# Optimization experiments

Measured on AMD Instinct MI355X. Metric: run time of the kernel, lower is better.

Reference implementation:

```python
import jax, jax.numpy as jnp
import numpy as np

N = 20000      # num nodes
E = 320000     # num edges
F = 128        # num_features
NUM_RBF = 20   # Message.num_atoms (hardcoded in torch source)
CUTOFF = 5.0


def setup_inputs() -> dict:
    key = jax.random.key(0)
    ks = jax.random.split(key, 12)
    node_s = jax.random.normal(ks[0], (N, F), dtype=jnp.float32)
    node_vec = jax.random.normal(ks[1], (N, F, 3), dtype=jnp.float32)
    edge = jax.random.randint(ks[2], (E, 2), 0, N, dtype=jnp.int32)
    edge_difference = jax.random.normal(ks[3], (E, 3), dtype=jnp.float32)
    # distances strictly positive and mostly inside cutoff (rbf divides by dist)
    edge_dis = jax.random.uniform(ks[4], (E,), dtype=jnp.float32, minval=0.5, maxval=CUTOFF * 1.1)
    s = 1.0 / np.sqrt(F)
    W1 = jax.random.normal(ks[5], (F, F), dtype=jnp.float32) * s
    b1 = jnp.zeros((F,), dtype=jnp.float32)
    W2 = jax.random.normal(ks[6], (F, 3 * F), dtype=jnp.float32) * s
    b2 = jnp.zeros((3 * F,), dtype=jnp.float32)
    Wf = jax.random.normal(ks[7], (NUM_RBF, 3 * F), dtype=jnp.float32) / np.sqrt(NUM_RBF)
    bf = jnp.zeros((3 * F,), dtype=jnp.float32)
    return {"node_s": node_s, "node_vec": node_vec, "edge": edge,
            "edge_difference": edge_difference, "edge_dis": edge_dis,
            "W1": W1, "b1": b1, "W2": W2, "b2": b2, "Wf": Wf, "bf": bf}


def reference(node_s, node_vec, edge, edge_difference, edge_dis, W1, b1, W2, b2, Wf, bf):
    src = edge[:, 1]  # gather index (neighbor j)
    dst = edge[:, 0]  # scatter index (center i)
    inv_d = 1.0 / edge_dis[:, None]                                   # [E,1]
    n = jnp.arange(1, NUM_RBF + 1, dtype=edge_dis.dtype)              # [20]
    rbf_feat = jnp.sin((n * (jnp.pi / CUTOFF)) * edge_dis[:, None]) * inv_d  # [E,20]
    filt = rbf_feat @ Wf + bf                                         # [E,3F]
    ccut = jnp.where(edge_dis <= CUTOFF,
                     0.5 * (jnp.cos(jnp.pi * edge_dis / CUTOFF) + 1.0), 0.0)  # [E]
    # faithful to torch: both filter and cutoff are re-indexed by edge[:,1]
    filter_W = filt[src] * ccut[src][:, None]                         # [E,3F]
    h = jax.nn.silu(node_s @ W1 + b1)                                 # [N,F]
    s_out = h @ W2 + b2                                               # [N,3F]
    filer_output = filter_W * s_out[src]                              # [E,3F]
    gate_state, gate_edge, message_scalar = jnp.split(filer_output, 3, axis=1)
    message_vec = node_vec[src] * gate_state[:, :, None]              # [E,F,3]
    # edge_vec in the torch source is dead code (never used) -> omitted
    temp_s = jnp.zeros_like(node_s).at[dst].add(message_scalar)       # [N,F]
    temp_vec = jnp.zeros_like(node_vec).at[dst].add(message_vec)      # [N,F,3]
    return (node_vec + temp_vec, node_s + temp_s)
```

## Files before the change

### kernel.cpp

```cpp
#include <hip/hip_runtime.h>
#include <hip/hip_bf16.h>

#define FDIM 128
#define NRBF 20
#define PI_OVER_CUT 0.6283185307179586f

#define WCONV_ELEMS (128 * 128 + 256 * 128 + 256 * 32)
#define WCONV_BLOCKS (WCONV_ELEMS / 256)

#define DEG_CAP 64

#define EPB 1024

typedef short bf8_t __attribute__((ext_vector_type(8)));
typedef float f4_t  __attribute__((ext_vector_type(4)));
typedef unsigned short us8_t __attribute__((ext_vector_type(8)));

static __device__ __forceinline__ unsigned short bf16_bits(float x) {
    unsigned u = __float_as_uint(x);
    unsigned r = u + 0x7FFF + ((u >> 16) & 1);
    return (unsigned short)(r >> 16);
}
static __device__ __forceinline__ float bf16_f(unsigned short b) {
    return __uint_as_float(((unsigned)b) << 16);
}

__global__ __launch_bounds__(256) void prep_kernel(
    const float* __restrict__ W1, const float* __restrict__ W2,
    const float* __restrict__ Wf,
    unsigned short* __restrict__ W1T, unsigned short* __restrict__ W2T,
    unsigned short* __restrict__ WfT,
    int* __restrict__ cursor, int N)
{
    int b = blockIdx.x;
    if (b < WCONV_BLOCKS) {
        int i = b * 256 + threadIdx.x;
        if (i < 128 * 128) {
            int n = i >> 7, k = i & 127;
            W1T[n * 128 + k] = bf16_bits(W1[k * 128 + n]);
        } else if (i < 128 * 128 + 256 * 128) {
            int j = i - 128 * 128;
            int n = j >> 7, k = j & 127;
            int col = (n < 128) ? n : n + 128;
            W2T[n * 128 + k] = bf16_bits(W2[k * 384 + col]);
        } else {
            int j = i - (128 * 128 + 256 * 128);
            int n = j >> 5, k = j & 31;
            int col = (n < 128) ? n : n + 128;
            WfT[n * 32 + k] = (k < NRBF) ? bf16_bits(Wf[k * 384 + col])
                                         : (unsigned short)0;
        }
    } else {
        int i = (b - WCONV_BLOCKS) * 256 + threadIdx.x;
        if (i < N) cursor[i] = 0;
    }
}

__global__ __launch_bounds__(256) void node_fused(
    const float* __restrict__ S, const float* __restrict__ node_vec,
    const float* __restrict__ edge_dis,
    const unsigned short* __restrict__ W1T, const float* __restrict__ b1,
    const unsigned short* __restrict__ W2T, const float* __restrict__ b2,
    const unsigned short* __restrict__ WfT, const float* __restrict__ bfv,
    ushort4* __restrict__ VM, int N,
    const int* __restrict__ edge, int* __restrict__ cursor,
    int* __restrict__ src_pad, int E, int edgeBlocks)
{
    if (blockIdx.x < edgeBlocks) {
        int base = blockIdx.x * EPB;
        #pragma unroll
        for (int it = 0; it < 4; it++) {
            int i = base + it * 256 + threadIdx.x;
            if (i < E) {
                int2 e = ((const int2*)edge)[i];
                int pos = atomicAdd(&cursor[e.x], 1);
                src_pad[((size_t)e.x << 6) + pos] = e.y;
            }
        }
        return;
    }

    __shared__ __align__(16) unsigned short sh_s[16][136];
    __shared__ __align__(16) unsigned short sh_h[16][136];
    __shared__ __align__(16) unsigned short sh_rbf[16][40];
    __shared__ float sh_ccut[16];

    const int tid  = threadIdx.x;
    const int lane = tid & 63;
    const int wave = tid >> 6;
    const int l15  = lane & 15;
    const int quad = lane >> 4;
    const int m0   = (blockIdx.x - edgeBlocks) * 16;

    for (int t = tid; t < 16 * 32; t += 256) {
        int row = t >> 5, c4 = (t & 31) * 4;
        int n = m0 + row; if (n >= N) n = N - 1;
        float4 x = *(const float4*)(S + (size_t)n * FDIM + c4);
        ushort4 u;
        u.x = bf16_bits(x.x); u.y = bf16_bits(x.y);
        u.z = bf16_bits(x.z); u.w = bf16_bits(x.w);
        *(ushort4*)&sh_s[row][c4] = u;
    }
    if (tid < 16 * 8) {
        int row = tid >> 3, k0 = (tid & 7) * 4;
        int n = m0 + row; if (n >= N) n = N - 1;
        float dd = edge_dis[n];
        float ph = PI_OVER_CUT * dd;
        float inv = 1.0f / dd;
        ushort4 u;
        u.x = (k0 + 0 < NRBF) ? bf16_bits(sinf((float)(k0 + 1) * ph) * inv) : 0;
        u.y = (k0 + 1 < NRBF) ? bf16_bits(sinf((float)(k0 + 2) * ph) * inv) : 0;
        u.z = (k0 + 2 < NRBF) ? bf16_bits(sinf((float)(k0 + 3) * ph) * inv) : 0;
        u.w = (k0 + 3 < NRBF) ? bf16_bits(sinf((float)(k0 + 4) * ph) * inv) : 0;
        *(ushort4*)&sh_rbf[row][k0] = u;
    }
    if (tid < 16) {
        int n = m0 + tid; if (n >= N) n = N - 1;
        float dd = edge_dis[n];
        sh_ccut[tid] = (dd <= 5.0f) ? 0.5f * (cosf(PI_OVER_CUT * dd) + 1.0f) : 0.0f;
    }
    __syncthreads();

    {
        bf8_t a1[4];
        #pragma unroll
        for (int kk = 0; kk < 4; kk++)
            a1[kk] = *(const bf8_t*)&sh_s[l15][kk * 32 + quad * 8];

        #pragma unroll
        for (int i = 0; i < 2; i++) {
            int col = (wave * 2 + i) * 16 + l15;
            const unsigned short* wp = W1T + (size_t)col * FDIM + quad * 8;
            f4_t acc = {0.f, 0.f, 0.f, 0.f};
            #pragma unroll
            for (int kk = 0; kk < 4; kk++) {
                bf8_t b = *(const bf8_t*)(wp + kk * 32);
                acc = __builtin_amdgcn_mfma_f32_16x16x32_bf16(a1[kk], b, acc, 0, 0, 0);
            }
            float bb = b1[col];
            #pragma unroll
            for (int r = 0; r < 4; r++) {
                float x = acc[r] + bb;
                x = x / (1.f + expf(-x));
                sh_h[quad * 4 + r][col] = bf16_bits(x);
            }
        }
    }
    __syncthreads();

    bf8_t a2[4], af;
    #pragma unroll
    for (int kk = 0; kk < 4; kk++)
        a2[kk] = *(const bf8_t*)&sh_h[l15][kk * 32 + quad * 8];
    af = *(const bf8_t*)&sh_rbf[l15][quad * 8];

    #pragma unroll
    for (int i = 0; i < 2; i++) {
        int pc = (wave * 2 + i) * 16 + l15;
        const unsigned short* wg = W2T + (size_t)pc * FDIM + quad * 8;
        const unsigned short* wm = W2T + (size_t)(pc + 128) * FDIM + quad * 8;
        f4_t ag = {0.f, 0.f, 0.f, 0.f}, am = {0.f, 0.f, 0.f, 0.f};
        #pragma unroll
        for (int kk = 0; kk < 4; kk++) {
            bf8_t bg = *(const bf8_t*)(wg + kk * 32);
            bf8_t bm = *(const bf8_t*)(wm + kk * 32);
            ag = __builtin_amdgcn_mfma_f32_16x16x32_bf16(a2[kk], bg, ag, 0, 0, 0);
            am = __builtin_amdgcn_mfma_f32_16x16x32_bf16(a2[kk], bm, am, 0, 0, 0);
        }
        f4_t fg = {0.f, 0.f, 0.f, 0.f}, fm = {0.f, 0.f, 0.f, 0.f};
        {
            bf8_t bg = *(const bf8_t*)(WfT + (size_t)pc * 32 + quad * 8);
            bf8_t bm = *(const bf8_t*)(WfT + (size_t)(pc + 128) * 32 + quad * 8);
            fg = __builtin_amdgcn_mfma_f32_16x16x32_bf16(af, bg, fg, 0, 0, 0);
            fm = __builtin_amdgcn_mfma_f32_16x16x32_bf16(af, bm, fm, 0, 0, 0);
        }

        float b2g = b2[pc], b2m = b2[256 + pc];
        float bfg = bfv[pc], bfm = bfv[256 + pc];
        #pragma unroll
        for (int r = 0; r < 4; r++) {
            int lrow = quad * 4 + r;
            int n = m0 + lrow;
            if (n < N) {
                float cc = sh_ccut[lrow];
                float a  = (fg[r] + bfg) * cc * (ag[r] + b2g);
                float mv = (fm[r] + bfm) * cc * (am[r] + b2m);
                const float* vp = node_vec + (size_t)n * 384 + 3 * pc;
                ushort4 rec;
                rec.x = bf16_bits(a * vp[0]);
                rec.y = bf16_bits(a * vp[1]);
                rec.z = bf16_bits(a * vp[2]);
                rec.w = bf16_bits(mv);
                VM[(size_t)n * FDIM + pc] = rec;
            }
        }
    }
}

__global__ __launch_bounds__(256) void gather_bf16(
    const int* __restrict__ cursor, const int* __restrict__ src_pad,
    const us8_t* __restrict__ VM8, const float* __restrict__ node_vec,
    const float* __restrict__ node_s,
    float* __restrict__ out_vec, float* __restrict__ out_s, int N)
{
    const int lane = threadIdx.x & 63;
    const int nw = gridDim.x * 4;
    for (int d = blockIdx.x * 4 + (threadIdx.x >> 6); d < N; d += nw) {
        int beg = d << 6;
        int end = beg + cursor[d];

        float a0A = 0.f, a1A = 0.f, a2A = 0.f, asA = 0.f;
        float a0B = 0.f, a1B = 0.f, a2B = 0.f, asB = 0.f;

        int j = beg;
        for (; j + 7 < end; j += 8) {
            us8_t r0 = VM8[(size_t)src_pad[j]     * 64 + lane];
            us8_t r1 = VM8[(size_t)src_pad[j + 1] * 64 + lane];
            us8_t r2 = VM8[(size_t)src_pad[j + 2] * 64 + lane];
            us8_t r3 = VM8[(size_t)src_pad[j + 3] * 64 + lane];
            us8_t r4 = VM8[(size_t)src_pad[j + 4] * 64 + lane];
            us8_t r5 = VM8[(size_t)src_pad[j + 5] * 64 + lane];
            us8_t r6 = VM8[(size_t)src_pad[j + 6] * 64 + lane];
            us8_t r7 = VM8[(size_t)src_pad[j + 7] * 64 + lane];
            #define ACC(r) \
                a0A += bf16_f(r[0]); a1A += bf16_f(r[1]); a2A += bf16_f(r[2]); asA += bf16_f(r[3]); \
                a0B += bf16_f(r[4]); a1B += bf16_f(r[5]); a2B += bf16_f(r[6]); asB += bf16_f(r[7]);
            ACC(r0) ACC(r1) ACC(r2) ACC(r3) ACC(r4) ACC(r5) ACC(r6) ACC(r7)
        }
        for (; j + 3 < end; j += 4) {
            us8_t r0 = VM8[(size_t)src_pad[j]     * 64 + lane];
            us8_t r1 = VM8[(size_t)src_pad[j + 1] * 64 + lane];
            us8_t r2 = VM8[(size_t)src_pad[j + 2] * 64 + lane];
            us8_t r3 = VM8[(size_t)src_pad[j + 3] * 64 + lane];
            ACC(r0) ACC(r1) ACC(r2) ACC(r3)
        }
        for (; j < end; j++) {
            us8_t r = VM8[(size_t)src_pad[j] * 64 + lane];
            ACC(r)
            #undef ACC
        }

        {
            const float* sp = node_s + (size_t)d * FDIM + 2 * lane;
            float* op = out_s + (size_t)d * FDIM + 2 * lane;
            float2 ns = *(const float2*)sp;
            float2 r; r.x = ns.x + asA; r.y = ns.y + asB;
            *(float2*)op = r;
        }
        {
            const float* ip = node_vec + (size_t)d * 384 + 6 * lane;
            float* op = out_vec + (size_t)d * 384 + 6 * lane;
            op[0] = ip[0] + a0A;
            op[1] = ip[1] + a1A;
            op[2] = ip[2] + a2A;
            op[3] = ip[3] + a0B;
            op[4] = ip[4] + a1B;
            op[5] = ip[5] + a2B;
        }
    }
}

extern "C" void kernel_launch(void* const* d_in, const int* in_sizes, int n_in,
                              void* d_out, int out_size, void* d_ws, size_t ws_size,
                              hipStream_t stream) {
    const float* node_s   = (const float*)d_in[0];
    const float* node_vec = (const float*)d_in[1];
    const int*   edge     = (const int*)d_in[2];
    const float* edge_dis = (const float*)d_in[4];
    const float* W1 = (const float*)d_in[5];
    const float* b1 = (const float*)d_in[6];
    const float* W2 = (const float*)d_in[7];
    const float* b2 = (const float*)d_in[8];
    const float* Wf = (const float*)d_in[9];
    const float* bf = (const float*)d_in[10];

    const int N = in_sizes[0] / FDIM;
    const int E = in_sizes[2] / 2;

    float* out_vec = (float*)d_out;
    float* out_s   = out_vec + (size_t)N * 384;

    int* cursor  = (int*)d_ws;
    int* src_pad = cursor + N;
    size_t int_bytes = (((size_t)N * (DEG_CAP + 1) * 4) + 15) & ~(size_t)15;
    unsigned short* W1T = (unsigned short*)((char*)d_ws + int_bytes);
    unsigned short* W2T = W1T + 128 * 128;
    unsigned short* WfT = W2T + 256 * 128;
    ushort4*        VMh = (ushort4*)(WfT + 256 * 32);

    const int zeroBlocks = (N + 255) / 256;
    prep_kernel<<<WCONV_BLOCKS + zeroBlocks, 256, 0, stream>>>(
        W1, W2, Wf, W1T, W2T, WfT, cursor, N);

    const int nodeBlocks = (N + 15) / 16;
    const int edgeBlocks = (E + EPB - 1) / EPB;
    node_fused<<<edgeBlocks + nodeBlocks, 256, 0, stream>>>(
        node_s, node_vec, edge_dis, W1T, b1, W2T, b2, WfT, bf, VMh, N,
        edge, cursor, src_pad, E, edgeBlocks);

    int gblocks = (N + 3) / 4;
    if (gblocks > 2048) gblocks = 2048;
    gather_bf16<<<gblocks, 256, 0, stream>>>(
        cursor, src_pad, (const us8_t*)VMh, node_vec, node_s,
        out_vec, out_s, N);
}
```

Measured before the change: 194.8 us.

## Merge prep, node and gather kernels into one cooperative persistent kernel

```diff
diff --git a/kernel.cpp b/kernel.cpp
--- a/kernel.cpp
+++ b/kernel.cpp
@@ -1,5 +1,8 @@
 #include <hip/hip_runtime.h>
+#include <hip/hip_cooperative_groups.h>
 #include <hip/hip_bf16.h>
+
+namespace cg = cooperative_groups;
 
 #define FDIM 128
 #define NRBF 20
@@ -25,72 +28,71 @@
     return __uint_as_float(((unsigned)b) << 16);
 }
 
-__global__ __launch_bounds__(256) void prep_kernel(
+struct NodeShared {
+    alignas(16) unsigned short sh_s[16][136];
+    alignas(16) unsigned short sh_h[16][136];
+    alignas(16) unsigned short sh_rbf[16][40];
+    alignas(16) float sh_ccut[16];
+};
+
+
+static __device__ __forceinline__ void do_prep_elem(
+    int i,
     const float* __restrict__ W1, const float* __restrict__ W2,
     const float* __restrict__ Wf,
     unsigned short* __restrict__ W1T, unsigned short* __restrict__ W2T,
     unsigned short* __restrict__ WfT,
     int* __restrict__ cursor, int N)
 {
-    int b = blockIdx.x;
-    if (b < WCONV_BLOCKS) {
-        int i = b * 256 + threadIdx.x;
-        if (i < 128 * 128) {
-            int n = i >> 7, k = i & 127;
-            W1T[n * 128 + k] = bf16_bits(W1[k * 128 + n]);
-        } else if (i < 128 * 128 + 256 * 128) {
-            int j = i - 128 * 128;
-            int n = j >> 7, k = j & 127;
-            int col = (n < 128) ? n : n + 128;
-            W2T[n * 128 + k] = bf16_bits(W2[k * 384 + col]);
-        } else {
-            int j = i - (128 * 128 + 256 * 128);
-            int n = j >> 5, k = j & 31;
-            int col = (n < 128) ? n : n + 128;
-            WfT[n * 32 + k] = (k < NRBF) ? bf16_bits(Wf[k * 384 + col])
-                                         : (unsigned short)0;
-        }
+    if (i < 128 * 128) {
+        int n = i >> 7, k = i & 127;
+        W1T[n * 128 + k] = bf16_bits(W1[k * 128 + n]);
+    } else if (i < 128 * 128 + 256 * 128) {
+        int j = i - 128 * 128;
+        int n = j >> 7, k = j & 127;
+        int col = (n < 128) ? n : n + 128;
+        W2T[n * 128 + k] = bf16_bits(W2[k * 384 + col]);
+    } else if (i < WCONV_ELEMS) {
+        int j = i - (128 * 128 + 256 * 128);
+        int n = j >> 5, k = j & 31;
+        int col = (n < 128) ? n : n + 128;
+        WfT[n * 32 + k] = (k < NRBF) ? bf16_bits(Wf[k * 384 + col])
+                                     : (unsigned short)0;
     } else {
-        int i = (b - WCONV_BLOCKS) * 256 + threadIdx.x;
-        if (i < N) cursor[i] = 0;
-    }
-}
-
-__global__ __launch_bounds__(256) void node_fused(
+        int d = i - WCONV_ELEMS;
+        if (d < N) cursor[d] = 0;
+    }
+}
+
+static __device__ __forceinline__ void do_edge_chunk(
+    int base, const int* __restrict__ edge, int E,
+    int* __restrict__ cursor, int* __restrict__ src_pad)
+{
+    #pragma unroll
+    for (int it = 0; it < 4; it++) {
+        int i = base + it * 256 + threadIdx.x;
+        if (i < E) {
+            int2 e = ((const int2*)edge)[i];
+            int pos = atomicAdd(&cursor[e.x], 1);
+            src_pad[((size_t)e.x << 6) + pos] = e.y;
+        }
+    }
+}
+
+static __device__ __forceinline__ void do_node_tile(
+    int m0, NodeShared& sh,
     const float* __restrict__ S, const float* __restrict__ node_vec,
     const float* __restrict__ edge_dis,
     const unsigned short* __restrict__ W1T, const float* __restrict__ b1,
     const unsigned short* __restrict__ W2T, const float* __restrict__ b2,
     const unsigned short* __restrict__ WfT, const float* __restrict__ bfv,
-    ushort4* __restrict__ VM, int N,
-    const int* __restrict__ edge, int* __restrict__ cursor,
-    int* __restrict__ src_pad, int E, int edgeBlocks)
-{
-    if (blockIdx.x < edgeBlocks) {
-        int base = blockIdx.x * EPB;
-        #pragma unroll
-        for (int it = 0; it < 4; it++) {
-            int i = base + it * 256 + threadIdx.x;
-            if (i < E) {
-                int2 e = ((const int2*)edge)[i];
-                int pos = atomicAdd(&cursor[e.x], 1);
-                src_pad[((size_t)e.x << 6) + pos] = e.y;
-            }
-        }
-        return;
-    }
-
-    __shared__ __align__(16) unsigned short sh_s[16][136];
-    __shared__ __align__(16) unsigned short sh_h[16][136];
-    __shared__ __align__(16) unsigned short sh_rbf[16][40];
-    __shared__ float sh_ccut[16];
-
+    ushort4* __restrict__ VM, int N)
+{
     const int tid  = threadIdx.x;
     const int lane = tid & 63;
     const int wave = tid >> 6;
     const int l15  = lane & 15;
     const int quad = lane >> 4;
-    const int m0   = (blockIdx.x - edgeBlocks) * 16;
 
     for (int t = tid; t < 16 * 32; t += 256) {
         int row = t >> 5, c4 = (t & 31) * 4;
@@ -99,7 +101,7 @@
         ushort4 u;
         u.x = bf16_bits(x.x); u.y = bf16_bits(x.y);
         u.z = bf16_bits(x.z); u.w = bf16_bits(x.w);
-        *(ushort4*)&sh_s[row][c4] = u;
+        *(ushort4*)&sh.sh_s[row][c4] = u;
     }
     if (tid < 16 * 8) {
         int row = tid >> 3, k0 = (tid & 7) * 4;
@@ -112,12 +114,12 @@
         u.y = (k0 + 1 < NRBF) ? bf16_bits(sinf((float)(k0 + 2) * ph) * inv) : 0;
         u.z = (k0 + 2 < NRBF) ? bf16_bits(sinf((float)(k0 + 3) * ph) * inv) : 0;
         u.w = (k0 + 3 < NRBF) ? bf16_bits(sinf((float)(k0 + 4) * ph) * inv) : 0;
-        *(ushort4*)&sh_rbf[row][k0] = u;
+        *(ushort4*)&sh.sh_rbf[row][k0] = u;
     }
     if (tid < 16) {
         int n = m0 + tid; if (n >= N) n = N - 1;
         float dd = edge_dis[n];
-        sh_ccut[tid] = (dd <= 5.0f) ? 0.5f * (cosf(PI_OVER_CUT * dd) + 1.0f) : 0.0f;
+        sh.sh_ccut[tid] = (dd <= 5.0f) ? 0.5f * (cosf(PI_OVER_CUT * dd) + 1.0f) : 0.0f;
     }
     __syncthreads();
 
@@ -125,7 +127,7 @@
         bf8_t a1[4];
         #pragma unroll
         for (int kk = 0; kk < 4; kk++)
-            a1[kk] = *(const bf8_t*)&sh_s[l15][kk * 32 + quad * 8];
+            a1[kk] = *(const bf8_t*)&sh.sh_s[l15][kk * 32 + quad * 8];
 
         #pragma unroll
         for (int i = 0; i < 2; i++) {
@@ -142,7 +144,7 @@
             for (int r = 0; r < 4; r++) {
                 float x = acc[r] + bb;
                 x = x / (1.f + expf(-x));
-                sh_h[quad * 4 + r][col] = bf16_bits(x);
+                sh.sh_h[quad * 4 + r][col] = bf16_bits(x);
             }
         }
     }
@@ -151,8 +153,8 @@
     bf8_t a2[4], af;
     #pragma unroll
     for (int kk = 0; kk < 4; kk++)
-        a2[kk] = *(const bf8_t*)&sh_h[l15][kk * 32 + quad * 8];
-    af = *(const bf8_t*)&sh_rbf[l15][quad * 8];
+        a2[kk] = *(const bf8_t*)&sh.sh_h[l15][kk * 32 + quad * 8];
+    af = *(const bf8_t*)&sh.sh_rbf[l15][quad * 8];
 
     #pragma unroll
     for (int i = 0; i < 2; i++) {
@@ -182,7 +184,7 @@
             int lrow = quad * 4 + r;
             int n = m0 + lrow;
             if (n < N) {
-                float cc = sh_ccut[lrow];
+                float cc = sh.sh_ccut[lrow];
                 float a  = (fg[r] + bfg) * cc * (ag[r] + b2g);
                 float mv = (fm[r] + bfm) * cc * (am[r] + b2m);
                 const float* vp = node_vec + (size_t)n * 384 + 3 * pc;
@@ -197,15 +199,16 @@
     }
 }
 
-__global__ __launch_bounds__(256) void gather_bf16(
+static __device__ __forceinline__ void do_gather(
+    int blockId, int nBlocks,
     const int* __restrict__ cursor, const int* __restrict__ src_pad,
     const us8_t* __restrict__ VM8, const float* __restrict__ node_vec,
     const float* __restrict__ node_s,
     float* __restrict__ out_vec, float* __restrict__ out_s, int N)
 {
     const int lane = threadIdx.x & 63;
-    const int nw = gridDim.x * 4;
-    for (int d = blockIdx.x * 4 + (threadIdx.x >> 6); d < N; d += nw) {
+    const int nw = nBlocks * 4;
+    for (int d = blockId * 4 + (threadIdx.x >> 6); d < N; d += nw) {
         int beg = d << 6;
         int end = beg + cursor[d];
 
@@ -260,6 +263,87 @@
     }
 }
 
+__global__ __launch_bounds__(256, 8) void mega_kernel(
+    const float* __restrict__ S, const float* __restrict__ node_vec,
+    const float* __restrict__ edge_dis,
+    const float* __restrict__ W1, const float* __restrict__ b1,
+    const float* __restrict__ W2, const float* __restrict__ b2,
+    const float* __restrict__ Wf, const float* __restrict__ bfv,
+    const int* __restrict__ edge,
+    unsigned short* __restrict__ W1T, unsigned short* __restrict__ W2T,
+    unsigned short* __restrict__ WfT,
+    int* __restrict__ cursor, int* __restrict__ src_pad,
+    ushort4* __restrict__ VM,
+    float* __restrict__ out_vec, float* __restrict__ out_s,
+    int N, int E)
+{
+    __shared__ NodeShared sh;
+    cg::grid_group grid = cg::this_grid();
+    const int gB = gridDim.x;
+
+    for (int i = blockIdx.x * 256 + threadIdx.x; i < WCONV_ELEMS + N; i += gB * 256)
+        do_prep_elem(i, W1, W2, Wf, W1T, W2T, WfT, cursor, N);
+    __threadfence();
+    grid.sync();
+
+    const int edgeBlocks = (E + EPB - 1) / EPB;
+    const int nodeBlocks = (N + 15) / 16;
+    for (int wb = blockIdx.x; wb < edgeBlocks + nodeBlocks; wb += gB) {
+        if (wb < edgeBlocks)
+            do_edge_chunk(wb * EPB, edge, E, cursor, src_pad);
+        else
+            do_node_tile((wb - edgeBlocks) * 16, sh, S, node_vec, edge_dis,
+                         W1T, b1, W2T, b2, WfT, bfv, VM, N);
+        __syncthreads();
+    }
+    __threadfence();
+    grid.sync();
+
+    do_gather(blockIdx.x, gB, cursor, src_pad, (const us8_t*)VM,
+              node_vec, S, out_vec, out_s, N);
+}
+
+__global__ __launch_bounds__(256) void prep_kernel(
+    const float* __restrict__ W1, const float* __restrict__ W2,
+    const float* __restrict__ Wf,
+    unsigned short* __restrict__ W1T, unsigned short* __restrict__ W2T,
+    unsigned short* __restrict__ WfT,
+    int* __restrict__ cursor, int N)
+{
+    int i = blockIdx.x * 256 + threadIdx.x;
+    if (i < WCONV_ELEMS + N)
+        do_prep_elem(i, W1, W2, Wf, W1T, W2T, WfT, cursor, N);
+}
+
+__global__ __launch_bounds__(256) void node_fused(
+    const float* __restrict__ S, const float* __restrict__ node_vec,
+    const float* __restrict__ edge_dis,
+    const unsigned short* __restrict__ W1T, const float* __restrict__ b1,
+    const unsigned short* __restrict__ W2T, const float* __restrict__ b2,
+    const unsigned short* __restrict__ WfT, const float* __restrict__ bfv,
+    ushort4* __restrict__ VM, int N,
+    const int* __restrict__ edge, int* __restrict__ cursor,
+    int* __restrict__ src_pad, int E, int edgeBlocks)
+{
+    if (blockIdx.x < edgeBlocks) {
+        do_edge_chunk(blockIdx.x * EPB, edge, E, cursor, src_pad);
+        return;
+    }
+    __shared__ NodeShared sh;
+    do_node_tile((blockIdx.x - edgeBlocks) * 16, sh, S, node_vec, edge_dis,
+                 W1T, b1, W2T, b2, WfT, bfv, VM, N);
+}
+
+__global__ __launch_bounds__(256) void gather_bf16(
+    const int* __restrict__ cursor, const int* __restrict__ src_pad,
+    const us8_t* __restrict__ VM8, const float* __restrict__ node_vec,
+    const float* __restrict__ node_s,
+    float* __restrict__ out_vec, float* __restrict__ out_s, int N)
+{
+    do_gather(blockIdx.x, gridDim.x, cursor, src_pad, VM8,
+              node_vec, node_s, out_vec, out_s, N);
+}
+
 extern "C" void kernel_launch(void* const* d_in, const int* in_sizes, int n_in,
                               void* d_out, int out_size, void* d_ws, size_t ws_size,
                               hipStream_t stream) {
@@ -274,8 +358,8 @@
     const float* Wf = (const float*)d_in[9];
     const float* bf = (const float*)d_in[10];
 
-    const int N = in_sizes[0] / FDIM;
-    const int E = in_sizes[2] / 2;
+    int N = in_sizes[0] / FDIM;
+    int E = in_sizes[2] / 2;
 
     float* out_vec = (float*)d_out;
     float* out_s   = out_vec + (size_t)N * 384;
@@ -288,8 +372,35 @@
     unsigned short* WfT = W2T + 256 * 128;
     ushort4*        VMh = (ushort4*)(WfT + 256 * 32);
 
-    const int zeroBlocks = (N + 255) / 256;
-    prep_kernel<<<WCONV_BLOCKS + zeroBlocks, 256, 0, stream>>>(
+    static int coopGrid = -2;
+    if (coopGrid == -2) {
+        int perCU = 0;
+        if (hipOccupancyMaxActiveBlocksPerMultiprocessor(
+                &perCU, mega_kernel, 256, 0) != hipSuccess)
+            perCU = 0;
+        if (perCU >= 4) {
+            int g = perCU * 256;
+            coopGrid = (g > 2048) ? 2048 : g;
+        } else {
+            coopGrid = 0;
+        }
+    }
+    if (coopGrid > 0) {
+        void* args[] = {
+            (void*)&node_s, (void*)&node_vec, (void*)&edge_dis,
+            (void*)&W1, (void*)&b1, (void*)&W2, (void*)&b2,
+            (void*)&Wf, (void*)&bf, (void*)&edge,
+            (void*)&W1T, (void*)&W2T, (void*)&WfT,
+            (void*)&cursor, (void*)&src_pad, (void*)&VMh,
+            (void*)&out_vec, (void*)&out_s, (void*)&N, (void*)&E };
+        hipError_t e = hipLaunchCooperativeKernel(
+            mega_kernel, dim3(coopGrid), dim3(256), args, 0, stream);
+        if (e == hipSuccess) return;
+        coopGrid = 0;
+    }
+
+    const int prepBlocks = (WCONV_ELEMS + N + 255) / 256;
+    prep_kernel<<<prepBlocks, 256, 0, stream>>>(
         W1, W2, Wf, W1T, W2T, WfT, cursor, N);
 
     const int nodeBlocks = (N + 15) / 16;
```

After: 605.9 us. 211% more time.
